# Performance work log

Measured on AMD Instinct MI355X. Metric: run time of the kernel, lower is better.

The kernel has to match this reference:

```python
import jax, jax.numpy as jnp
import numpy as np

# SSFM configuration (matches init_kwargs; amplification/noise disabled)
ALPHA = 0.046       # attenuation [1/km]
BETA2 = -21.67      # GVD [ps^2/km]
GAMMA = 1.27        # nonlinearity [1/km/W]
LENGTH = 80.0       # fiber length [km]
N_SSFM = 64         # number of SSFM steps
HALF_WIN = 100      # half Hamming window length
DT = 1.0            # normalized sample duration


def _make_window(n):
    # tf.signal.hamming_window(2*HALF_WIN) is periodic: 0.54 - 0.46*cos(2*pi*k/L)
    L = 2 * HALF_WIN
    w = (0.54 - 0.46 * jnp.cos(2.0 * np.float32(np.pi) * jnp.arange(L, dtype=jnp.float32) / np.float32(L)))
    win = jnp.concatenate([w[:HALF_WIN], jnp.ones((n - L,), jnp.float32), w[HALF_WIN:]])
    return win.astype(jnp.complex64)


def _freq_vector(n):
    # sionna.utils.time_frequency_vector: f = (arange(n) - n/2) / (n * dt)
    return ((jnp.arange(n, dtype=jnp.float32) - np.float32(n / 2)) / np.float32(n * DT))


def setup_inputs() -> dict:
    key = jax.random.key(0)
    k1, k2 = jax.random.split(key)
    shape = (4, 262144)
    x_real = 0.05 * jax.random.normal(k1, shape, dtype=jnp.float32)
    x_imag = 0.05 * jax.random.normal(k2, shape, dtype=jnp.float32)
    return {"x_real": x_real, "x_imag": x_imag}


def reference(x_real, x_imag):
    x = (x_real + 1j * x_imag).astype(jnp.complex64)  # [B, N]
    n = x.shape[-1]
    f = _freq_vector(n)                                # [N]
    win = _make_window(n)                              # [N] complex
    dz = np.float32(LENGTH / N_SSFM)

    def apply_linear(q, dz_):
        # dispersion: exp(-j * beta2/2 * dz * (2*pi*f)^2), fftshifted
        phase = -(np.float32(BETA2) / 2.0) * dz_ * (2.0 * np.float32(np.pi) * f) ** 2
        disp = jnp.fft.fftshift(jnp.exp(1j * phase).astype(jnp.complex64))
        q = jnp.fft.ifft(jnp.fft.fft(q, axis=-1) * disp, axis=-1)
        # attenuation
        q = q * jnp.exp(np.float32(-ALPHA / 2.0) * dz_).astype(jnp.complex64)
        return q

    def apply_nonlinear(q, dz_):
        phi = (jnp.abs(q) ** 2) * np.float32(GAMMA) * (-dz_)
        return q * jnp.exp(1j * phi)

    # symmetrized SSFM: D(dz/2) [W N(dz) D(dz)]^{n-1} W N(dz) D(dz/2)
    q = apply_linear(x, dz / 2.0)

    def step(q, _):
        q = q * win
        q = apply_nonlinear(q, dz)
        q = apply_linear(q, dz)
        return q, None

    q, _ = jax.lax.scan(step, q, None, length=N_SSFM - 1)

    q = q * win
    q = apply_nonlinear(q, dz)
    q = apply_linear(q, dz / 2.0)

    # return real/imag stacked so the output is a real tensor: [2, B, N]
    return jnp.stack([jnp.real(q), jnp.imag(q)], axis=0)
```

## Files before the change

kernel.cpp:

```cpp
#include <hip/hip_runtime.h>


static constexpr double PI_D = 3.14159265358979323846;

__device__ __forceinline__ float2 cadd(float2 a, float2 b){ return make_float2(a.x+b.x, a.y+b.y); }
__device__ __forceinline__ float2 csub(float2 a, float2 b){ return make_float2(a.x-b.x, a.y-b.y); }
__device__ __forceinline__ float2 cmul(float2 a, float2 b){
  return make_float2(fmaf(a.x, b.x, -(a.y*b.y)), fmaf(a.x, b.y, a.y*b.x));
}
__device__ __forceinline__ float2 cmulc(float2 a, float2 b){
  return make_float2(fmaf(a.x, b.x, a.y*b.y), fmaf(a.y, b.x, -(a.x*b.y)));
}

__device__ __forceinline__ float2 ldg_dev(const float2* p){
  unsigned long long v = __hip_atomic_load((const unsigned long long*)p,
                                           __ATOMIC_RELAXED, __HIP_MEMORY_SCOPE_AGENT);
  union { unsigned long long u; float2 f; } cv; cv.u = v; return cv.f;
}
__device__ __forceinline__ void stg_dev(float2* p, float2 v){
  union { unsigned long long u; float2 f; } cv; cv.f = v;
  __hip_atomic_store((unsigned long long*)p, cv.u,
                     __ATOMIC_RELAXED, __HIP_MEMORY_SCOPE_AGENT);
}

__device__ __forceinline__ int sg(int e){
  int d2 = (e>>6)&7, d1 = (e>>3)&7;
  return e ^ (d2<<3) ^ d1 ^ d2;
}

template<int INV>
__device__ __forceinline__ void dft8(float2 r[8]){
  const float RS = 0.7071067811865476f;
  float2 t0=cadd(r[0],r[4]), t4=csub(r[0],r[4]);
  float2 t1=cadd(r[1],r[5]), t5=csub(r[1],r[5]);
  float2 t2=cadd(r[2],r[6]), t6=csub(r[2],r[6]);
  float2 t3=cadd(r[3],r[7]), t7=csub(r[3],r[7]);
  float2 u1,u2,u3;
  if(!INV){
    u1 = make_float2((t5.x+t5.y)*RS, (t5.y-t5.x)*RS);
    u2 = make_float2(t6.y, -t6.x);
    u3 = make_float2((t7.y-t7.x)*RS, -(t7.x+t7.y)*RS);
  } else {
    u1 = make_float2((t5.x-t5.y)*RS, (t5.x+t5.y)*RS);
    u2 = make_float2(-t6.y, t6.x);
    u3 = make_float2(-(t7.x+t7.y)*RS, (t7.x-t7.y)*RS);
  }
  float2 e0=cadd(t0,t2), e1=csub(t0,t2), e2=cadd(t1,t3), e3=csub(t1,t3);
  float2 f3 = (!INV)? make_float2(e3.y,-e3.x) : make_float2(-e3.y,e3.x);
  r[0]=cadd(e0,e2); r[4]=csub(e0,e2); r[2]=cadd(e1,f3); r[6]=csub(e1,f3);
  float2 o0=cadd(t4,u2), o1=csub(t4,u2), o2=cadd(u1,u3), o3=csub(u1,u3);
  float2 g3 = (!INV)? make_float2(o3.y,-o3.x) : make_float2(-o3.y,o3.x);
  r[1]=cadd(o0,o2); r[5]=csub(o0,o2); r[3]=cadd(o1,g3); r[7]=csub(o1,g3);
}

__device__ __forceinline__ void fwd512(float2 r[8], int l, int p, int j,
                                       const float2* t1, const float2* t2, float2* ex){
  dft8<0>(r);
  #pragma unroll
  for(int q=1;q<8;q++) r[q]=cmul(r[q],t1[q-1]);
  #pragma unroll
  for(int q=0;q<8;q++) ex[sg(l+64*q)] = r[q];
  #pragma unroll
  for(int m=0;m<8;m++) r[m] = ex[sg(64*j+p+8*m)];
  dft8<0>(r);
  #pragma unroll
  for(int q=1;q<8;q++) r[q]=cmul(r[q],t2[q-1]);
  #pragma unroll
  for(int q=0;q<8;q++) ex[sg(64*j+p+8*q)] = r[q];
  #pragma unroll
  for(int m=0;m<8;m++) r[m] = ex[sg(64*j+8*p+m)];
  dft8<0>(r);
}
__device__ __forceinline__ void inv512(float2 r[8], int l, int p, int j,
                                       const float2* t1, const float2* t2, float2* ex){
  dft8<1>(r);
  #pragma unroll
  for(int m=0;m<8;m++) ex[sg(64*j+8*p+m)] = r[m];
  #pragma unroll
  for(int q=0;q<8;q++) r[q] = ex[sg(64*j+p+8*q)];
  #pragma unroll
  for(int q=1;q<8;q++) r[q]=cmulc(r[q],t2[q-1]);
  dft8<1>(r);
  #pragma unroll
  for(int m=0;m<8;m++) ex[sg(64*j+p+8*m)] = r[m];
  #pragma unroll
  for(int q=0;q<8;q++) r[q] = ex[sg(l+64*q)];
  #pragma unroll
  for(int q=1;q<8;q++) r[q]=cmulc(r[q],t1[q-1]);
  dft8<1>(r);
}

template<int INV>
__device__ __forceinline__ void fft512(float2 r[8], int l, float2* ex){
  const float W512 = (float)(2.0*PI_D/512.0);
  const float W64  = (float)(2.0*PI_D/64.0);
  int j = l>>3, p = l&7;
  float s,c;
  if(!INV){
    dft8<0>(r);
    __sincosf(-W512*(float)l, &s, &c);
    float2 w = make_float2(c,s), cur = w;
    #pragma unroll
    for(int q=1;q<8;q++){ r[q]=cmul(r[q],cur); cur=cmul(cur,w); }
    #pragma unroll
    for(int q=0;q<8;q++) ex[sg(l + 64*q)] = r[q];
    #pragma unroll
    for(int m=0;m<8;m++) r[m] = ex[sg(64*j + p + 8*m)];
    dft8<0>(r);
    __sincosf(-W64*(float)p, &s, &c);
    w = make_float2(c,s); cur = w;
    #pragma unroll
    for(int q=1;q<8;q++){ r[q]=cmul(r[q],cur); cur=cmul(cur,w); }
    #pragma unroll
    for(int q=0;q<8;q++) ex[sg(64*j + p + 8*q)] = r[q];
    #pragma unroll
    for(int m=0;m<8;m++) r[m] = ex[sg(64*j + 8*p + m)];
    dft8<0>(r);
  } else {
    dft8<1>(r);
    #pragma unroll
    for(int m=0;m<8;m++) ex[sg(64*j + 8*p + m)] = r[m];
    #pragma unroll
    for(int q=0;q<8;q++) r[q] = ex[sg(64*j + p + 8*q)];
    __sincosf(W64*(float)p, &s, &c);
    float2 w = make_float2(c,s), cur = w;
    #pragma unroll
    for(int q=1;q<8;q++){ r[q]=cmul(r[q],cur); cur=cmul(cur,w); }
    dft8<1>(r);
    #pragma unroll
    for(int m=0;m<8;m++) ex[sg(64*j + p + 8*m)] = r[m];
    #pragma unroll
    for(int q=0;q<8;q++) r[q] = ex[sg(l + 64*q)];
    __sincosf(W512*(float)l, &s, &c);
    w = make_float2(c,s); cur = w;
    #pragma unroll
    for(int q=1;q<8;q++){ r[q]=cmul(r[q],cur); cur=cmul(cur,w); }
    dft8<1>(r);
  }
}

__global__ __launch_bounds__(512) void kSetup(float2* __restrict__ dispF, float2* __restrict__ dispH,
                                              int* __restrict__ bar){
  int m  = blockIdx.x*512 + threadIdx.x;
  if (m < 16384) bar[m] = 0;
  int k1 = m >> 9, k2 = m & 511;
  int k  = k1 + (k2 << 9);
  int ks = (k < 131072) ? k : k - 262144;
  float fv  = (float)ks / 262144.0f;
  float tpf = 6.28318548202514648f * fv;
  float e2  = tpf * tpf;
  const float bh = 10.8350000381469727f;
  float phF = (bh * 1.25f)  * e2;
  float phH = (bh * 0.625f) * e2;
  double sF,cF,sH,cH;
  sincos((double)phF, &sF, &cF);
  sincos((double)phH, &sH, &cH);
  const float aco = -0.023000000044703484f;
  double scF = exp((double)(aco*1.25f))  / 262144.0;
  double scH = exp((double)(aco*0.625f)) / 262144.0;
  dispF[m] = make_float2((float)(cF*scF), (float)(sF*scF));
  dispH[m] = make_float2((float)(cH*scH), (float)(sH*scH));
}

__global__ __launch_bounds__(512) void kA(const float2* __restrict__ src, float2* __restrict__ dst,
                                          const float2* __restrict__ disp){
  __shared__ float2 ex[8][512];
  int t = threadIdx.x, w = t>>6, l = t&63;
  int k1 = blockIdx.x*8 + w;
  size_t base = ((size_t)blockIdx.y<<18) + (size_t)k1*512;
  const float2* s = src + base;
  float2* d = dst + base;
  float2 r[8];
  #pragma unroll
  for(int m=0;m<8;m++) r[m] = s[l + 64*m];
  fft512<0>(r, l, ex[w]);
  int p=l&7, j=l>>3;
  const float2* dp = disp + (size_t)k1*512;
  #pragma unroll
  for(int q=0;q<8;q++) r[q] = cmul(r[q], dp[64*q + 8*p + j]);
  fft512<1>(r, l, ex[w]);
  float c1 = (float)(2.0*PI_D/262144.0)*(float)k1;
  float sb,cb,ss,cs;
  __sincosf(c1*(float)l, &sb, &cb);
  __sincosf(c1*64.0f,    &ss, &cs);
  float2 tw = make_float2(cb,sb), st = make_float2(cs,ss);
  #pragma unroll
  for(int m=0;m<8;m++){ d[l+64*m] = cmul(r[m], tw); tw = cmul(tw, st); }
}

template<int MODE>
__global__ __launch_bounds__(512) void kB(const float* __restrict__ xr, const float* __restrict__ xi,
                                          const float2* __restrict__ src, float2* __restrict__ dst,
                                          float* __restrict__ outp){
  __shared__ float2 tile[8][514];
  int t=threadIdx.x, w=t>>6, l=t&63;
  int c0 = blockIdx.x*8;
  size_t base = ((size_t)blockIdx.y<<18);
  #pragma unroll
  for(int i=0;i<8;i++){
    int rr = i*64 + (t>>3), cc = t&7;
    size_t a = base + (size_t)rr*512 + (size_t)(c0 + cc);
    if(MODE==0) tile[cc][sg(rr)] = make_float2(xr[a], xi[a]);
    else        tile[cc][sg(rr)] = src[a];
  }
  __syncthreads();
  float2 r[8];
  int p=l&7, j=l>>3;
  int n2 = c0 + w;
  if(MODE==0){
    #pragma unroll
    for(int m=0;m<8;m++) r[m] = tile[w][sg(l + 64*m)];
  } else {
    #pragma unroll
    for(int q=0;q<8;q++) r[q] = tile[w][sg(64*q + 8*p + j)];
    fft512<1>(r, l, tile[w]);
  }
  if(MODE==1){
    #pragma unroll
    for(int m=0;m<8;m++){
      int n1 = l + 64*m;
      float wv = 1.0f;
      if(n1==0 && n2<100){
        float ang = (6.28318548202514648f*(float)n2)*0.005f;
        wv = 0.54f - 0.46f*cosf(ang);
      } else if(n1==511 && n2>=412){
        float ang = (6.28318548202514648f*(float)(n2-312))*0.005f;
        wv = 0.54f - 0.46f*cosf(ang);
      }
      float2 qv = make_float2(r[m].x*wv, r[m].y*wv);
      float aq2 = fmaf(qv.x,qv.x, qv.y*qv.y);
      float phi = (aq2 * 1.26999998092651367f) * (-1.25f);
      float sp,cp; __sincosf(phi,&sp,&cp);
      r[m] = cmul(qv, make_float2(cp,sp));
    }
  }
  if(MODE==2){
    #pragma unroll
    for(int m=0;m<8;m++) tile[w][sg(l + 64*m)] = r[m];
    __syncthreads();
    #pragma unroll
    for(int i=0;i<8;i++){
      int rr = i*64 + (t>>3), cc = t&7;
      float2 v = tile[cc][sg(rr)];
      size_t a = base + (size_t)rr*512 + (size_t)(c0 + cc);
      outp[a] = v.x;
      outp[(size_t)(1<<20) + a] = v.y;
    }
    return;
  }
  fft512<0>(r, l, tile[w]);
  float c1 = -(float)(2.0*PI_D/262144.0)*(float)n2;
  float sb,cb,ss,cs;
  __sincosf(c1*(float)(8*p + j), &sb, &cb);
  __sincosf(c1*64.0f,            &ss, &cs);
  float2 tw=make_float2(cb,sb), st=make_float2(cs,ss);
  #pragma unroll
  for(int q=0;q<8;q++){ r[q]=cmul(r[q],tw); tw=cmul(tw,st); }
  #pragma unroll
  for(int q=0;q<8;q++) tile[w][sg(64*q + 8*p + j)] = r[q];
  __syncthreads();
  #pragma unroll
  for(int i=0;i<8;i++){
    int rr = i*64 + (t>>3), cc = t&7;
    dst[base + (size_t)rr*512 + (size_t)(c0 + cc)] = tile[cc][sg(rr)];
  }
}

__device__ __forceinline__ void gsync(int* bar, int slotbase, int phase){
  __syncthreads();
  if (threadIdx.x == 0){
    int* cnt = bar + slotbase + phase*16;
    __hip_atomic_fetch_add(cnt, 1, __ATOMIC_RELAXED, __HIP_MEMORY_SCOPE_AGENT);
    while (__hip_atomic_load(cnt, __ATOMIC_RELAXED, __HIP_MEMORY_SCOPE_AGENT) != 64)
      __builtin_amdgcn_s_sleep(1);
    asm volatile("" ::: "memory");
  }
  __syncthreads();
}

__global__ __launch_bounds__(512, 1) void ssfm_all(
    const float* __restrict__ xr, const float* __restrict__ xi,
    float* __restrict__ outp,
    float2* __restrict__ buf1, float2* __restrict__ buf2,
    const float2* __restrict__ dispF, const float2* __restrict__ dispH,
    int* __restrict__ bar)
{
  __shared__ float2 tile[8][514];
  const int t=threadIdx.x, w=t>>6, l=t&63, p=l&7, j=l>>3;
  const int bi=blockIdx.x;
  const int lb=((bi&7)<<5)|(bi>>3);
  const int b=lb>>6, g=lb&63;
  const size_t base=(size_t)b<<18;
  const int k1=g*8+w, c0=g*8, n2=c0+w;
  const int slotbase = b*140*16;
  float2* exch = tile[w];

  float2 t1[7], t2[7], dpF[8], dpH[8];
  #pragma unroll
  for(int q=1;q<8;q++){
    double s,c;
    sincos(-2.0*PI_D*(double)(l*q)/512.0,&s,&c); t1[q-1]=make_float2((float)c,(float)s);
    sincos(-2.0*PI_D*(double)(p*q)/64.0,&s,&c);  t2[q-1]=make_float2((float)c,(float)s);
  }
  float2 baseA, stA, baseB, stB;
  {
    double s,c;
    sincos( 2.0*PI_D*(double)(k1*l)/262144.0,&s,&c);        baseA=make_float2((float)c,(float)s);
    sincos( 2.0*PI_D*(double)(k1*64)/262144.0,&s,&c);       stA  =make_float2((float)c,(float)s);
    sincos(-2.0*PI_D*(double)(n2*(8*p+j))/262144.0,&s,&c);  baseB=make_float2((float)c,(float)s);
    sincos(-2.0*PI_D*(double)(n2*64)/262144.0,&s,&c);       stB  =make_float2((float)c,(float)s);
  }
  #pragma unroll
  for(int q=0;q<8;q++){
    int di=k1*512+64*q+8*p+j;
    dpF[q]=dispF[di]; dpH[q]=dispH[di];
  }
  float wvH=1.0f, wvT=1.0f;
  if(l==0  && n2<100)  wvH=0.54f-0.46f*cosf((6.28318548202514648f*(float)n2)*0.005f);
  if(l==63 && n2>=412) wvT=0.54f-0.46f*cosf((6.28318548202514648f*(float)(n2-312))*0.005f);

  {
    #pragma unroll
    for(int i=0;i<8;i++){
      int rr=i*64+(t>>3), cc=t&7;
      size_t a=base+(size_t)rr*512+(size_t)(c0+cc);
      tile[cc][sg(rr)]=make_float2(xr[a], xi[a]);
    }
    __syncthreads();
    float2 r[8];
    #pragma unroll
    for(int m=0;m<8;m++) r[m]=exch[sg(l+64*m)];
    fwd512(r,l,p,j,t1,t2,exch);
    float2 tw=baseB;
    #pragma unroll
    for(int q=0;q<8;q++){ r[q]=cmul(r[q],tw); tw=cmul(tw,stB); }
    #pragma unroll
    for(int q=0;q<8;q++) exch[sg(64*q+8*p+j)]=r[q];
    __syncthreads();
    #pragma unroll
    for(int i=0;i<8;i++){
      int rr=i*64+(t>>3), cc=t&7;
      stg_dev(&buf1[base+(size_t)rr*512+(size_t)(c0+cc)], tile[cc][sg(rr)]);
    }
  }
  gsync(bar, slotbase, 0);
  {
    const size_t rowbase=base+(size_t)k1*512;
    float2 r[8];
    #pragma unroll
    for(int m=0;m<8;m++) r[m]=ldg_dev(&buf1[rowbase+l+64*m]);
    fwd512(r,l,p,j,t1,t2,exch);
    #pragma unroll
    for(int q=0;q<8;q++) r[q]=cmul(r[q],dpH[q]);
    inv512(r,l,p,j,t1,t2,exch);
    float2 tw=baseA;
    #pragma unroll
    for(int m=0;m<8;m++){ stg_dev(&buf2[rowbase+l+64*m], cmul(r[m],tw)); tw=cmul(tw,stA); }
  }
  gsync(bar, slotbase, 1);

  #pragma unroll 1
  for(int it=0; it<64; ++it){
    {
      #pragma unroll
      for(int i=0;i<8;i++){
        int rr=i*64+(t>>3), cc=t&7;
        tile[cc][sg(rr)]=ldg_dev(&buf2[base+(size_t)rr*512+(size_t)(c0+cc)]);
      }
      __syncthreads();
      float2 r[8];
      #pragma unroll
      for(int q=0;q<8;q++) r[q]=exch[sg(64*q+8*p+j)];
      inv512(r,l,p,j,t1,t2,exch);
      #pragma unroll
      for(int m=0;m<8;m++){
        float wv = (m==0)? wvH : ((m==7)? wvT : 1.0f);
        float2 qv=make_float2(r[m].x*wv, r[m].y*wv);
        float aq2=fmaf(qv.x,qv.x, qv.y*qv.y);
        float phi=(aq2*1.26999998092651367f)*(-1.25f);
        float sp,cp; __sincosf(phi,&sp,&cp);
        r[m]=cmul(qv,make_float2(cp,sp));
      }
      fwd512(r,l,p,j,t1,t2,exch);
      float2 tw=baseB;
      #pragma unroll
      for(int q=0;q<8;q++){ r[q]=cmul(r[q],tw); tw=cmul(tw,stB); }
      #pragma unroll
      for(int q=0;q<8;q++) exch[sg(64*q+8*p+j)]=r[q];
      __syncthreads();
      #pragma unroll
      for(int i=0;i<8;i++){
        int rr=i*64+(t>>3), cc=t&7;
        stg_dev(&buf1[base+(size_t)rr*512+(size_t)(c0+cc)], tile[cc][sg(rr)]);
      }
    }
    gsync(bar, slotbase, 2+2*it);
    {
      const size_t rowbase=base+(size_t)k1*512;
      float2 r[8];
      #pragma unroll
      for(int m=0;m<8;m++) r[m]=ldg_dev(&buf1[rowbase+l+64*m]);
      fwd512(r,l,p,j,t1,t2,exch);
      const bool lastH=(it==63);
      #pragma unroll
      for(int q=0;q<8;q++){ float2 dq = lastH? dpH[q] : dpF[q]; r[q]=cmul(r[q],dq); }
      inv512(r,l,p,j,t1,t2,exch);
      float2 tw=baseA;
      #pragma unroll
      for(int m=0;m<8;m++){ stg_dev(&buf2[rowbase+l+64*m], cmul(r[m],tw)); tw=cmul(tw,stA); }
    }
    gsync(bar, slotbase, 3+2*it);
  }

  {
    #pragma unroll
    for(int i=0;i<8;i++){
      int rr=i*64+(t>>3), cc=t&7;
      tile[cc][sg(rr)]=ldg_dev(&buf2[base+(size_t)rr*512+(size_t)(c0+cc)]);
    }
    __syncthreads();
    float2 r[8];
    #pragma unroll
    for(int q=0;q<8;q++) r[q]=exch[sg(64*q+8*p+j)];
    inv512(r,l,p,j,t1,t2,exch);
    #pragma unroll
    for(int m=0;m<8;m++) exch[sg(l+64*m)]=r[m];
    __syncthreads();
    #pragma unroll
    for(int i=0;i<8;i++){
      int rr=i*64+(t>>3), cc=t&7;
      float2 v=tile[cc][sg(rr)];
      size_t a=base+(size_t)rr*512+(size_t)(c0+cc);
      outp[a]=v.x;
      outp[(size_t)(1<<20)+a]=v.y;
    }
  }
}

extern "C" void kernel_launch(void* const* d_in, const int* in_sizes, int n_in,
                              void* d_out, int out_size, void* d_ws, size_t ws_size,
                              hipStream_t stream) {
  (void)in_sizes; (void)n_in; (void)out_size; (void)ws_size;
  const float* xr = (const float*)d_in[0];
  const float* xi = (const float*)d_in[1];
  float* out = (float*)d_out;
  char* ws = (char*)d_ws;
  float2* buf1  = (float2*)ws;
  float2* buf2  = (float2*)(ws + ((size_t)8<<20));
  float2* dispF = (float2*)(ws + ((size_t)16<<20));
  float2* dispH = (float2*)(ws + ((size_t)18<<20));
  int*    bar   = (int*)   (ws + ((size_t)20<<20));

  kSetup<<<dim3(512), dim3(512), 0, stream>>>(dispF, dispH, bar);

  void* args[] = {(void*)&xr,(void*)&xi,(void*)&out,(void*)&buf1,(void*)&buf2,
                  (void*)&dispF,(void*)&dispH,(void*)&bar};
  hipError_t e = hipLaunchCooperativeKernel((void*)ssfm_all, dim3(256), dim3(512),
                                            args, 0, stream);
  if (e != hipSuccess){
    dim3 blk(512), gdim(64,4);
    kB<0><<<gdim, blk, 0, stream>>>(xr, xi, nullptr, buf1, nullptr);
    kA<<<gdim, blk, 0, stream>>>(buf1, buf2, dispH);
    for(int i=0;i<63;i++){
      kB<1><<<gdim, blk, 0, stream>>>(nullptr, nullptr, buf2, buf1, nullptr);
      kA<<<gdim, blk, 0, stream>>>(buf1, buf2, dispF);
    }
    kB<1><<<gdim, blk, 0, stream>>>(nullptr, nullptr, buf2, buf1, nullptr);
    kA<<<gdim, blk, 0, stream>>>(buf1, buf2, dispH);
    kB<2><<<gdim, blk, 0, stream>>>(nullptr, nullptr, buf2, nullptr, out);
  }
}
```

Measured before the change: 1.639 ms.

## Use XCD-aware cache-coherence bits for inter-block exchange loads and stores

New measurement: 1.728 ms. 1.05x slower.

```diff
diff --git a/kernel.cpp b/kernel.cpp
--- a/kernel.cpp
+++ b/kernel.cpp
@@ -12,20 +12,29 @@
   return make_float2(fmaf(a.x, b.x, a.y*b.y), fmaf(a.y, b.x, -(a.x*b.y)));
 }
 
-__device__ __forceinline__ float2 ldg_dev(const float2* p){
-  unsigned long long v = __hip_atomic_load((const unsigned long long*)p,
-                                           __ATOMIC_RELAXED, __HIP_MEMORY_SCOPE_AGENT);
-  union { unsigned long long u; float2 f; } cv; cv.u = v; return cv.f;
-}
-__device__ __forceinline__ void stg_dev(float2* p, float2 v){
-  union { unsigned long long u; float2 f; } cv; cv.f = v;
-  __hip_atomic_store((unsigned long long*)p, cv.u,
-                     __ATOMIC_RELAXED, __HIP_MEMORY_SCOPE_AGENT);
-}
-
 __device__ __forceinline__ int sg(int e){
   int d2 = (e>>6)&7, d1 = (e>>3)&7;
   return e ^ (d2<<3) ^ d1 ^ d2;
+}
+
+__device__ __forceinline__ float2 u2f(unsigned long long u){ union{unsigned long long u; float2 f;}c; c.u=u; return c.f; }
+__device__ __forceinline__ unsigned long long f2u(float2 f){ union{unsigned long long u; float2 f;}c; c.f=f; return c.u; }
+
+__device__ __forceinline__ void gl_near(unsigned long long &d, unsigned long long bp, unsigned voff){
+  asm volatile("global_load_dwordx2 %0, %1, %2 sc0" : "=&v"(d) : "v"(voff), "s"(bp) : "memory");
+}
+__device__ __forceinline__ void gl_far(unsigned long long &d, unsigned long long bp, unsigned voff){
+  asm volatile("global_load_dwordx2 %0, %1, %2 sc0 sc1" : "=&v"(d) : "v"(voff), "s"(bp) : "memory");
+}
+__device__ __forceinline__ void gs_near(unsigned long long bp, unsigned voff, unsigned long long v){
+  asm volatile("global_store_dwordx2 %0, %1, %2" :: "v"(voff), "v"(v), "s"(bp) : "memory");
+}
+__device__ __forceinline__ void gs_far(unsigned long long bp, unsigned voff, unsigned long long v){
+  asm volatile("global_store_dwordx2 %0, %1, %2 sc0 sc1" :: "v"(voff), "v"(v), "s"(bp) : "memory");
+}
+__device__ __forceinline__ void vwait(){
+  asm volatile("s_waitcnt vmcnt(0)" ::: "memory");
+  __builtin_amdgcn_sched_barrier(0);
 }
 
 template<int INV>
@@ -267,6 +276,7 @@
 }
 
 __device__ __forceinline__ void gsync(int* bar, int slotbase, int phase){
+  asm volatile("s_waitcnt vmcnt(0)" ::: "memory");
   __syncthreads();
   if (threadIdx.x == 0){
     int* cnt = bar + slotbase + phase*16;
@@ -277,15 +287,28 @@
   }
   __syncthreads();
 }
+__device__ __forceinline__ void gsyncAll(int* bar){
+  asm volatile("s_waitcnt vmcnt(0)" ::: "memory");
+  __syncthreads();
+  if (threadIdx.x == 0){
+    int* cnt = bar + 9000;
+    __hip_atomic_fetch_add(cnt, 1, __ATOMIC_RELAXED, __HIP_MEMORY_SCOPE_AGENT);
+    while (__hip_atomic_load(cnt, __ATOMIC_RELAXED, __HIP_MEMORY_SCOPE_AGENT) != 256)
+      __builtin_amdgcn_s_sleep(1);
+    asm volatile("" ::: "memory");
+  }
+  __syncthreads();
+}
 
 __global__ __launch_bounds__(512, 1) void ssfm_all(
     const float* __restrict__ xr, const float* __restrict__ xi,
     float* __restrict__ outp,
     float2* __restrict__ buf1, float2* __restrict__ buf2,
     const float2* __restrict__ dispF, const float2* __restrict__ dispH,
-    int* __restrict__ bar)
+    int* __restrict__ bar, int* __restrict__ xcdtab)
 {
   __shared__ float2 tile[8][514];
+  __shared__ int sxcd[64];
   const int t=threadIdx.x, w=t>>6, l=t&63, p=l&7, j=l>>3;
   const int bi=blockIdx.x;
   const int lb=((bi&7)<<5)|(bi>>3);
@@ -294,6 +317,20 @@
   const int k1=g*8+w, c0=g*8, n2=c0+w;
   const int slotbase = b*140*16;
   float2* exch = tile[w];
+  const unsigned long long b1p=(unsigned long long)buf1, b2p=(unsigned long long)buf2;
+
+  int myx;
+  asm("s_getreg_b32 %0, hwreg(HW_REG_XCC_ID)" : "=s"(myx));
+  if (t==0)
+    __hip_atomic_store(&xcdtab[lb], myx, __ATOMIC_RELAXED, __HIP_MEMORY_SCOPE_AGENT);
+  gsyncAll(bar);
+  if (t<64)
+    sxcd[t] = __hip_atomic_load(&xcdtab[b*64+t], __ATOMIC_RELAXED, __HIP_MEMORY_SCOPE_AGENT);
+  __syncthreads();
+  int smask=0;
+  #pragma unroll
+  for(int i=0;i<8;i++) smask |= (sxcd[8*i+w]==myx) ? (1<<i) : 0;
+  smask = __builtin_amdgcn_readfirstlane(smask);
 
   float2 t1[7], t2[7], dpF[8], dpH[8];
   #pragma unroll
@@ -319,12 +356,16 @@
   if(l==0  && n2<100)  wvH=0.54f-0.46f*cosf((6.28318548202514648f*(float)n2)*0.005f);
   if(l==63 && n2>=412) wvT=0.54f-0.46f*cosf((6.28318548202514648f*(float)(n2-312))*0.005f);
 
+  const int cc8 = t&7, q8 = t>>3;
+  const unsigned voffB0 = (unsigned)(((size_t)base + (size_t)q8*512 + (size_t)(c0+cc8))*8);
+  const unsigned voffA0 = (unsigned)(((size_t)base + (size_t)(8*g+cc8)*512 + (size_t)q8)*8);
+
   {
     #pragma unroll
     for(int i=0;i<8;i++){
-      int rr=i*64+(t>>3), cc=t&7;
-      size_t a=base+(size_t)rr*512+(size_t)(c0+cc);
-      tile[cc][sg(rr)]=make_float2(xr[a], xi[a]);
+      int rr=i*64+q8;
+      size_t a=base+(size_t)rr*512+(size_t)(c0+cc8);
+      tile[cc8][sg(rr)]=make_float2(xr[a], xi[a]);
     }
     __syncthreads();
     float2 r[8];
@@ -337,36 +378,59 @@
     #pragma unroll
     for(int q=0;q<8;q++) exch[sg(64*q+8*p+j)]=r[q];
     __syncthreads();
-    #pragma unroll
-    for(int i=0;i<8;i++){
-      int rr=i*64+(t>>3), cc=t&7;
-      stg_dev(&buf1[base+(size_t)rr*512+(size_t)(c0+cc)], tile[cc][sg(rr)]);
+    unsigned voff=voffB0;
+    #pragma unroll
+    for(int i=0;i<8;i++){
+      unsigned long long v=f2u(tile[cc8][sg(i*64+q8)]);
+      if(smask&(1<<i)) gs_near(b1p,voff,v); else gs_far(b1p,voff,v);
+      voff += 262144u;
     }
   }
   gsync(bar, slotbase, 0);
   {
-    const size_t rowbase=base+(size_t)k1*512;
+    unsigned long long v[8]; unsigned voff=voffA0;
+    #pragma unroll
+    for(int i=0;i<8;i++){
+      if(smask&(1<<i)) gl_near(v[i],b1p,voff); else gl_far(v[i],b1p,voff);
+      voff += 512u;
+    }
+    vwait();
+    #pragma unroll
+    for(int i=0;i<8;i++) tile[cc8][sg(i*64+q8)] = u2f(v[i]);
+    __syncthreads();
     float2 r[8];
     #pragma unroll
-    for(int m=0;m<8;m++) r[m]=ldg_dev(&buf1[rowbase+l+64*m]);
+    for(int m=0;m<8;m++) r[m]=exch[sg(l+64*m)];
     fwd512(r,l,p,j,t1,t2,exch);
     #pragma unroll
     for(int q=0;q<8;q++) r[q]=cmul(r[q],dpH[q]);
     inv512(r,l,p,j,t1,t2,exch);
     float2 tw=baseA;
     #pragma unroll
-    for(int m=0;m<8;m++){ stg_dev(&buf2[rowbase+l+64*m], cmul(r[m],tw)); tw=cmul(tw,stA); }
+    for(int m=0;m<8;m++){ exch[sg(l+64*m)]=cmul(r[m],tw); tw=cmul(tw,stA); }
+    __syncthreads();
+    voff=voffA0;
+    #pragma unroll
+    for(int i=0;i<8;i++){
+      unsigned long long vv=f2u(tile[cc8][sg(i*64+q8)]);
+      if(smask&(1<<i)) gs_near(b2p,voff,vv); else gs_far(b2p,voff,vv);
+      voff += 512u;
+    }
   }
   gsync(bar, slotbase, 1);
 
   #pragma unroll 1
   for(int it=0; it<64; ++it){
     {
+      unsigned long long v[8]; unsigned voff=voffB0;
       #pragma unroll
       for(int i=0;i<8;i++){
-        int rr=i*64+(t>>3), cc=t&7;
-        tile[cc][sg(rr)]=ldg_dev(&buf2[base+(size_t)rr*512+(size_t)(c0+cc)]);
+        if(smask&(1<<i)) gl_near(v[i],b2p,voff); else gl_far(v[i],b2p,voff);
+        voff += 262144u;
       }
+      vwait();
+      #pragma unroll
+      for(int i=0;i<8;i++) tile[cc8][sg(i*64+q8)] = u2f(v[i]);
       __syncthreads();
       float2 r[8];
       #pragma unroll
@@ -388,18 +452,29 @@
       #pragma unroll
       for(int q=0;q<8;q++) exch[sg(64*q+8*p+j)]=r[q];
       __syncthreads();
+      voff=voffB0;
       #pragma unroll
       for(int i=0;i<8;i++){
-        int rr=i*64+(t>>3), cc=t&7;
-        stg_dev(&buf1[base+(size_t)rr*512+(size_t)(c0+cc)], tile[cc][sg(rr)]);
+        unsigned long long vv=f2u(tile[cc8][sg(i*64+q8)]);
+        if(smask&(1<<i)) gs_near(b1p,voff,vv); else gs_far(b1p,voff,vv);
+        voff += 262144u;
       }
     }
     gsync(bar, slotbase, 2+2*it);
     {
-      const size_t rowbase=base+(size_t)k1*512;
+      unsigned long long v[8]; unsigned voff=voffA0;
+      #pragma unroll
+      for(int i=0;i<8;i++){
+        if(smask&(1<<i)) gl_near(v[i],b1p,voff); else gl_far(v[i],b1p,voff);
+        voff += 512u;
+      }
+      vwait();
+      #pragma unroll
+      for(int i=0;i<8;i++) tile[cc8][sg(i*64+q8)] = u2f(v[i]);
+      __syncthreads();
       float2 r[8];
       #pragma unroll
-      for(int m=0;m<8;m++) r[m]=ldg_dev(&buf1[rowbase+l+64*m]);
+      for(int m=0;m<8;m++) r[m]=exch[sg(l+64*m)];
       fwd512(r,l,p,j,t1,t2,exch);
       const bool lastH=(it==63);
       #pragma unroll
@@ -407,17 +482,29 @@
       inv512(r,l,p,j,t1,t2,exch);
       float2 tw=baseA;
       #pragma unroll
-      for(int m=0;m<8;m++){ stg_dev(&buf2[rowbase+l+64*m], cmul(r[m],tw)); tw=cmul(tw,stA); }
+      for(int m=0;m<8;m++){ exch[sg(l+64*m)]=cmul(r[m],tw); tw=cmul(tw,stA); }
+      __syncthreads();
+      voff=voffA0;
+      #pragma unroll
+      for(int i=0;i<8;i++){
+        unsigned long long vv=f2u(tile[cc8][sg(i*64+q8)]);
+        if(smask&(1<<i)) gs_near(b2p,voff,vv); else gs_far(b2p,voff,vv);
+        voff += 512u;
+      }
     }
     gsync(bar, slotbase, 3+2*it);
   }
 
   {
-    #pragma unroll
-    for(int i=0;i<8;i++){
-      int rr=i*64+(t>>3), cc=t&7;
-      tile[cc][sg(rr)]=ldg_dev(&buf2[base+(size_t)rr*512+(size_t)(c0+cc)]);
-    }
+    unsigned long long v[8]; unsigned voff=voffB0;
+    #pragma unroll
+    for(int i=0;i<8;i++){
+      if(smask&(1<<i)) gl_near(v[i],b2p,voff); else gl_far(v[i],b2p,voff);
+      voff += 262144u;
+    }
+    vwait();
+    #pragma unroll
+    for(int i=0;i<8;i++) tile[cc8][sg(i*64+q8)] = u2f(v[i]);
     __syncthreads();
     float2 r[8];
     #pragma unroll
@@ -428,11 +515,11 @@
     __syncthreads();
     #pragma unroll
     for(int i=0;i<8;i++){
-      int rr=i*64+(t>>3), cc=t&7;
-      float2 v=tile[cc][sg(rr)];
-      size_t a=base+(size_t)rr*512+(size_t)(c0+cc);
-      outp[a]=v.x;
-      outp[(size_t)(1<<20)+a]=v.y;
+      int rr=i*64+q8;
+      float2 vv=tile[cc8][sg(rr)];
+      size_t a=base+(size_t)rr*512+(size_t)(c0+cc8);
+      outp[a]=vv.x;
+      outp[(size_t)(1<<20)+a]=vv.y;
     }
   }
 }
@@ -450,11 +537,12 @@
   float2* dispF = (float2*)(ws + ((size_t)16<<20));
   float2* dispH = (float2*)(ws + ((size_t)18<<20));
   int*    bar   = (int*)   (ws + ((size_t)20<<20));
+  int*    xcdt  = (int*)   (ws + ((size_t)21<<20));
 
   kSetup<<<dim3(512), dim3(512), 0, stream>>>(dispF, dispH, bar);
 
   void* args[] = {(void*)&xr,(void*)&xi,(void*)&out,(void*)&buf1,(void*)&buf2,
-                  (void*)&dispF,(void*)&dispH,(void*)&bar};
+                  (void*)&dispF,(void*)&dispH,(void*)&bar,(void*)&xcdt};
   hipError_t e = hipLaunchCooperativeKernel((void*)ssfm_all, dim3(256), dim3(512),
                                             args, 0, stream);
   if (e != hipSuccess){
```
